# Kernel optimization log

Measured on AMD Instinct MI355X. Metric: run time of the kernel, lower is better.

The kernel has to match this reference:

```python
import jax, jax.numpy as jnp
import numpy as np

B, L, D = 8, 2048, 256
D_MODEL = 1024
NUM_SIGNALS = 16
MAX_POSITIONS = 4096
ROLE_OUTPUT = 2  # role id used for the CLS token


def setup_inputs() -> dict:
    key = jax.random.key(0)
    ks = jax.random.split(key, 12)
    emb = jax.random.normal(ks[0], (B, L, D), dtype=jnp.float32)
    pos = jax.random.randint(ks[1], (B, L), 1, MAX_POSITIONS + 1)          # pos >= 1 for real tokens
    sid = jax.random.randint(ks[2], (B, L), 0, NUM_SIGNALS)
    role = jax.random.randint(ks[3], (B, L), 0, 3)
    padding_mask = jax.random.uniform(ks[4], (B, L)) < 0.75                # True = real token
    # learned parameters
    proj_W = jax.random.normal(ks[5], (NUM_SIGNALS, D_MODEL, D), dtype=jnp.float32) * (1.0 / np.sqrt(D))
    proj_b = jax.random.normal(ks[6], (NUM_SIGNALS, D_MODEL), dtype=jnp.float32) * 0.01
    cls_content = jax.random.normal(ks[7], (D_MODEL,), dtype=jnp.float32)
    pos_embed = jax.random.normal(ks[8], (MAX_POSITIONS + 1, D_MODEL), dtype=jnp.float32)
    id_embed = jax.random.normal(ks[9], (NUM_SIGNALS + 1, D_MODEL), dtype=jnp.float32)
    role_embed = jax.random.normal(ks[10], (3, D_MODEL), dtype=jnp.float32)
    return dict(emb=emb, pos=pos, sid=sid, role=role, padding_mask=padding_mask,
                proj_W=proj_W, proj_b=proj_b, cls_content=cls_content,
                pos_embed=pos_embed, id_embed=id_embed, role_embed=role_embed)


def reference(emb, pos, sid, role, padding_mask,
              proj_W, proj_b, cls_content, pos_embed, id_embed, role_embed):
    Bv, Lv, _ = emb.shape
    S, d_model, _ = proj_W.shape
    cls_id = S

    # Grouped per-signal projection: one GEMM per signal id, select per token.
    tokens = jnp.zeros((Bv, Lv, d_model), dtype=emb.dtype)
    for s in range(S):
        proj_s = jnp.einsum('bld,ed->ble', emb, proj_W[s]) + proj_b[s]   # (B, L, d_model)
        keep = ((sid == s) & padding_mask)[..., None]
        tokens = jnp.where(keep, proj_s, tokens)

    # Prepend CLS
    cls = jnp.broadcast_to(cls_content[None, None, :], (Bv, 1, d_model))
    tokens = jnp.concatenate([cls, tokens], axis=1)                       # (B, L+1, d_model)

    pos_full = jnp.concatenate([jnp.zeros((Bv, 1), dtype=pos.dtype), pos], axis=1)
    sid_full = jnp.concatenate([jnp.full((Bv, 1), cls_id, dtype=sid.dtype), sid], axis=1)
    role_full = jnp.concatenate([jnp.full((Bv, 1), ROLE_OUTPUT, dtype=role.dtype), role], axis=1)

    tokens = tokens + pos_embed[pos_full] + id_embed[sid_full] + role_embed[role_full]

    attn_keep = jnp.concatenate([jnp.ones((Bv, 1), dtype=bool), padding_mask], axis=1)
    return tokens, attn_keep
```

## Files before the change

### kernel.cpp

```cpp
#include <hip/hip_runtime.h>
#include <hip/hip_bf16.h>
#include <stdint.h>

#define B_ 8
#define L_ 2048
#define NTOK 16384
#define DK 256
#define DM 1024
#define NS 16
#define LOUT 2049
#define TOK_OUT (B_*LOUT*DM)
#define ATTN_OUT (B_*LOUT)
#define PCAP 2048

typedef unsigned short u16;
typedef unsigned int u32;
typedef __bf16 bf16x8 __attribute__((ext_vector_type(8)));
typedef float f32x4 __attribute__((ext_vector_type(4)));

__device__ inline u32 packbf2(float lo, float hi) {
    u32 a, b;
    __builtin_memcpy(&a, &lo, 4);
    __builtin_memcpy(&b, &hi, 4);
    a = (a + 0x8000u) >> 16;
    b = (b + 0x8000u) & 0xFFFF0000u;
    return a | b;
}

__device__ inline void gll16(const void* g, void* l) {
    __builtin_amdgcn_global_load_lds(
        (const __attribute__((address_space(1))) unsigned int*)g,
        (__attribute__((address_space(3))) unsigned int*)l, 16, 0, 0);
}

#define WS_CUR 0
#define WS_PERM 64
#define EMB_OFF 262144ULL
#define W_OFF (EMB_OFF + 16384ULL * 512ULL)
#define WS_NEED (W_OFF + 16384ULL * 512ULL)

__device__ inline int sniff_width(const unsigned char* mb, int tid, int* sh) {
    if (tid == 0) { sh[0] = 0; sh[1] = 0; sh[2] = 0; }
    __syncthreads();
    int c1ge2 = 0, ge2 = 0, oddnz = 0;
    const u32* mw = (const u32*)mb;
    #pragma unroll
    for (int i = 0; i < 16; i++) {
        u32 x = mw[tid * 16 + i];
        u32 b0 = x & 0xFF, b1 = (x >> 8) & 0xFF, b2 = (x >> 16) & 0xFF, b3 = x >> 24;
        if (b1 >= 2) c1ge2 = 1;
        if (b0 >= 2 || b1 >= 2 || b2 >= 2 || b3 >= 2) ge2 = 1;
        if ((b1 | b3) != 0) oddnz = 1;
    }
    if (c1ge2) atomicOr(&sh[0], 1);
    if (ge2) atomicOr(&sh[1], 1);
    if (oddnz) atomicOr(&sh[2], 1);
    __syncthreads();
    if (sh[0]) return 2;
    if (sh[1]) return 4;
    if (sh[2]) return 1;
    return 4;
}

__device__ inline int decode_mask(const unsigned char* mb, int t, int width) {
    if (width == 1) return mb[t] != 0;
    if (width == 2) return ((const u16*)mb)[t] != 0;
    return ((const u32*)mb)[t] != 0;
}

#define SORT_B 64
#define CONV_B 2048
#define EW_B 4096
#define EW0 (SORT_B + CONV_B)
#define CLS0 (EW0 + EW_B)
#define ATTN0 (CLS0 + 2)
#define PREP_GRID (ATTN0 + 65)

__global__ __launch_bounds__(256) void prep_all(
    const unsigned char* __restrict__ mb, const int* __restrict__ sid,
    const int* __restrict__ pos, const int* __restrict__ role,
    const float* __restrict__ emb, const float* __restrict__ W,
    const float* __restrict__ cls, const float* __restrict__ pos_emb,
    const float* __restrict__ id_emb, const float* __restrict__ role_emb,
    int* __restrict__ wsi, unsigned char* __restrict__ wsb,
    float* __restrict__ out) {
    __shared__ int sh[3];
    __shared__ int lcnt[NS], gbase[NS];
    int bid = blockIdx.x;
    int tid = threadIdx.x;
    int lane = tid & 63;
    int wv = tid >> 6;

    if (bid < SORT_B) {
        if (tid < NS) lcnt[tid] = 0;
        int width = sniff_width(mb, tid, sh);
        int t = bid * 256 + tid;
        int m = decode_mask(mb, t, width);
        int s = sid[t];
        int lr = 0;
        if (m) lr = atomicAdd(&lcnt[s], 1);
        __syncthreads();
        if (tid < NS) gbase[tid] = atomicAdd(&wsi[WS_CUR + tid], lcnt[tid]);
        __syncthreads();
        if (m) {
            int r = gbase[s] + lr;
            if (r < PCAP) wsi[WS_PERM + s * PCAP + r] = t;
        }
        return;
    }

    if (bid < EW0) {
        int cb = bid - SORT_B;
        const float* src;
        u16* dst;
        if (cb < 1024) {
            src = emb;
            dst = (u16*)(wsb + EMB_OFF);
        } else {
            cb -= 1024;
            src = W;
            dst = (u16*)(wsb + W_OFF);
        }
        int r0 = cb * 16 + wv * 4;
        #pragma unroll
        for (int i = 0; i < 4; i++) {
            int r = r0 + i;
            float4 a = *(const float4*)(src + (size_t)r * DK + lane * 4);
            uint2 o;
            o.x = packbf2(a.x, a.y);
            o.y = packbf2(a.z, a.w);
            *(uint2*)(dst + (size_t)r * DK + lane * 4) = o;
        }
        return;
    }

    if (bid < CLS0) {
        int width = sniff_width(mb, tid, sh);
        int t = (bid - EW0) * 4 + wv;
        if (decode_mask(mb, t, width)) return;
        int p = pos[t], sd = sid[t], ro = role[t];
        int b = t >> 11, l = t & 2047;
        size_t orow = (size_t)(b * LOUT + l + 1) * DM;
        const float* pr = pos_emb + (size_t)p * DM;
        const float* ir = id_emb + (size_t)sd * DM;
        const float* rr = role_emb + (size_t)ro * DM;
        #pragma unroll
        for (int it = 0; it < 4; it++) {
            int c = it * 256 + lane * 4;
            f32x4 a = *(const f32x4*)(pr + c);
            f32x4 d = *(const f32x4*)(ir + c);
            f32x4 e = *(const f32x4*)(rr + c);
            f32x4 o = a + d + e;
            __builtin_nontemporal_store(o, (f32x4*)(out + orow + c));
        }
        return;
    }

    if (bid < ATTN0) {
        int b = (bid - CLS0) * 4 + wv;
        size_t orow = (size_t)(b * LOUT) * DM;
        #pragma unroll
        for (int it = 0; it < 4; it++) {
            int c = it * 256 + lane * 4;
            f32x4 cc = *(const f32x4*)(cls + c);
            f32x4 a = *(const f32x4*)(pos_emb + c);
            f32x4 d = *(const f32x4*)(id_emb + NS * DM + c);
            f32x4 e = *(const f32x4*)(role_emb + 2 * DM + c);
            f32x4 o = cc + a + d + e;
            *(f32x4*)(out + orow + c) = o;
        }
        return;
    }

    {
        int width = sniff_width(mb, tid, sh);
        int i = (bid - ATTN0) * 256 + tid;
        if (i < ATTN_OUT) {
            int b = i / LOUT;
            int j = i - b * LOUT;
            float val = (j == 0) ? 1.0f
                                 : (float)decode_mask(mb, b * L_ + j - 1, width);
            out[TOK_OUT + i] = val;
        }
    }
}

__global__ __launch_bounds__(512, 4) void gemm_big(
    const int* __restrict__ pos, const int* __restrict__ role,
    const float* __restrict__ bias,
    const float* __restrict__ pos_emb, const float* __restrict__ id_emb,
    const float* __restrict__ role_emb,
    const int* __restrict__ wsi, const unsigned char* __restrict__ wsb,
    float* __restrict__ out) {
    __shared__ u16 As[2][128 * 32];
    __shared__ u16 Bs[2][256 * 32];
    __shared__ int toks[128];
    int bi = (int)blockIdx.x;
    int tid = threadIdx.x;
    int lane = tid & 63;
    int wv = tid >> 6;

    int cnts[NS];
    int mtot = 0;
    #pragma unroll
    for (int i = 0; i < NS; i++) {
        int c = wsi[WS_CUR + i];
        cnts[i] = c > PCAP ? PCAP : c;
        mtot += (cnts[i] + 127) >> 7;
    }
    int xcd = bi & 7;
    int j = bi >> 3;
    int m_lo = (xcd * mtot) >> 3;
    int m_hi = ((xcd + 1) * mtot) >> 3;
    int cm = m_hi - m_lo;
    if (cm <= 0 || j >= cm * 4) return;
    int nt = j / cm;
    int m = m_lo + (j - nt * cm);
    int n0 = nt << 8;

    int s = -1, lrt = 0;
    #pragma unroll
    for (int i = 0; i < NS; i++) {
        int rt = (cnts[i] + 127) >> 7;
        if (s < 0) {
            if (m < rt) { s = i; lrt = m; }
            else m -= rt;
        }
    }
    if (s < 0) return;
    int rowsValid = cnts[s] - lrt * 128;
    if (rowsValid > 128) rowsValid = 128;

    if (tid < 128) {
        int base = WS_PERM + s * PCAP + lrt * 128;
        toks[tid] = wsi[base + ((tid < rowsValid) ? tid : 0)];
    }
    __syncthreads();

    const u16* Eb = (const u16*)(wsb + EMB_OFF);
    const u16* Bb = (const u16*)(wsb + W_OFF) + (size_t)(s * DM + n0) * DK;

    int srow = lane >> 2;
    int slseg = lane & 3;
    int arow = wv * 16 + srow;
    int ags = (slseg - (arow >> 1)) & 3;
    int brow1 = 128 + arow;
    int bgs1 = (slseg - (brow1 >> 1)) & 3;
    const u16* Asrc = Eb + (size_t)toks[arow] * DK;

    f32x4 acc[4][4];
    #pragma unroll
    for (int im = 0; im < 4; im++)
        #pragma unroll
        for (int jn = 0; jn < 4; jn++) acc[im][jn] = (f32x4){0.f, 0.f, 0.f, 0.f};

    int wm = wv & 1, wn = wv >> 1;
    int mcol = lane & 15;
    int quad = lane >> 4;

#define STAGE(kc, bf)                                                          \
    {                                                                          \
        gll16(Asrc + (kc) * 32 + ags * 8, &As[bf][wv * 16 * 32]);              \
        gll16(Bb + (size_t)arow * DK + (kc) * 32 + ags * 8,                    \
              &Bs[bf][wv * 16 * 32]);                                          \
        gll16(Bb + (size_t)brow1 * DK + (kc) * 32 + bgs1 * 8,                  \
              &Bs[bf][(128 + wv * 16) * 32]);                                  \
    }

    STAGE(0, 0)
    #pragma unroll
    for (int kc = 0; kc < 8; ++kc) {
        __syncthreads();
        if (kc < 7) STAGE(kc + 1, (kc + 1) & 1)
        int bf = kc & 1;
        bf16x8 af[4], bfr[4];
        #pragma unroll
        for (int im = 0; im < 4; im++) {
            int row = wm * 64 + im * 16 + mcol;
            int sg = (quad + (row >> 1)) & 3;
            af[im] = *(const bf16x8*)(&As[bf][row * 32 + sg * 8]);
        }
        #pragma unroll
        for (int jn = 0; jn < 4; jn++) {
            int row = wn * 64 + jn * 16 + mcol;
            int sg = (quad + (row >> 1)) & 3;
            bfr[jn] = *(const bf16x8*)(&Bs[bf][row * 32 + sg * 8]);
        }
        #pragma unroll
        for (int im = 0; im < 4; im++)
            #pragma unroll
            for (int jn = 0; jn < 4; jn++)
                acc[im][jn] = __builtin_amdgcn_mfma_f32_16x16x32_bf16(
                    af[im], bfr[jn], acc[im][jn], 0, 0, 0);
    }

    float bc[4];
    #pragma unroll
    for (int jn = 0; jn < 4; jn++) {
        int col = n0 + wn * 64 + jn * 16 + mcol;
        bc[jn] = bias[s * DM + col] + id_emb[s * DM + col];
    }
    #pragma unroll
    for (int im = 0; im < 4; im++) {
        #pragma unroll
        for (int r = 0; r < 4; r++) {
            int rowT = wm * 64 + im * 16 + quad * 4 + r;
            if (rowT >= rowsValid) continue;
            int t = toks[rowT];
            int p = pos[t];
            int ro = role[t];
            int b = t >> 11, l = t & 2047;
            size_t orow = (size_t)(b * LOUT + l + 1) * DM;
            const float* prow = pos_emb + (size_t)p * DM;
            #pragma unroll
            for (int jn = 0; jn < 4; jn++) {
                int col = n0 + wn * 64 + jn * 16 + mcol;
                float val = acc[im][jn][r] + bc[jn]
                    + prow[col]
                    + role_emb[ro * DM + col];
                __builtin_nontemporal_store(val, &out[orow + col]);
            }
        }
    }
#undef STAGE
}

extern "C" void kernel_launch(void* const* d_in, const int* in_sizes, int n_in,
                              void* d_out, int out_size, void* d_ws, size_t ws_size,
                              hipStream_t stream) {
    const float* emb = (const float*)d_in[0];
    const int* pos = (const int*)d_in[1];
    const int* sid = (const int*)d_in[2];
    const int* role = (const int*)d_in[3];
    const unsigned char* mask = (const unsigned char*)d_in[4];
    const float* W = (const float*)d_in[5];
    const float* bias = (const float*)d_in[6];
    const float* cls = (const float*)d_in[7];
    const float* pos_emb = (const float*)d_in[8];
    const float* id_emb = (const float*)d_in[9];
    const float* role_emb = (const float*)d_in[10];
    float* out = (float*)d_out;
    int* wsi = (int*)d_ws;
    unsigned char* wsb = (unsigned char*)d_ws;

    (void)hipMemsetAsync(wsi, 0, 64 * sizeof(int), stream);
    hipLaunchKernelGGL(prep_all, dim3(PREP_GRID), dim3(256), 0, stream,
                       mask, sid, pos, role, emb, W, cls, pos_emb, id_emb,
                       role_emb, wsi, wsb, out);
    hipLaunchKernelGGL(gemm_big, dim3(576), dim3(512), 0, stream,
                       pos, role, bias, pos_emb, id_emb, role_emb,
                       wsi, wsb, out);
}
```

Before: 156.6 us.

## Move unmasked-token, CLS and attn-mask writes from prep kernel into GEMM kernel tail

The sort phase now also builds a compacted list of padded (unmasked) token indices and records the detected mask width in the workspace. The elementwise writes for padded tokens, CLS rows and the attention mask move out of the prep kernel and into the tail of the GEMM kernel, which idle or finished GEMM blocks process in a grid-stride loop. The prep kernel shrinks to sorting plus bf16 conversion, now done with fewer, larger blocks of 64 rows each. The aim is to overlap the memory-bound embedding writes with the GEMM and shorten the prep critical path, at the cost of longer tails on GEMM blocks and a capacity limit (UCAP) on the padded-token list.

```diff
diff --git a/kernel.cpp b/kernel.cpp
--- a/kernel.cpp
+++ b/kernel.cpp
@@ -12,6 +12,7 @@
 #define TOK_OUT (B_*LOUT*DM)
 #define ATTN_OUT (B_*LOUT)
 #define PCAP 2048
+#define UCAP 8192
 
 typedef unsigned short u16;
 typedef unsigned int u32;
@@ -34,7 +35,10 @@
 }
 
 #define WS_CUR 0
+#define WS_UCUR 16
+#define WS_WIDTH 32
 #define WS_PERM 64
+#define WS_UNM (64 + NS * PCAP)
 #define EMB_OFF 262144ULL
 #define W_OFF (EMB_OFF + 16384ULL * 512ULL)
 #define WS_NEED (W_OFF + 16384ULL * 512ULL)
@@ -69,23 +73,15 @@
 }
 
 #define SORT_B 64
-#define CONV_B 2048
-#define EW_B 4096
-#define EW0 (SORT_B + CONV_B)
-#define CLS0 (EW0 + EW_B)
-#define ATTN0 (CLS0 + 2)
-#define PREP_GRID (ATTN0 + 65)
+#define PREP_GRID (SORT_B + 512)
 
 __global__ __launch_bounds__(256) void prep_all(
     const unsigned char* __restrict__ mb, const int* __restrict__ sid,
-    const int* __restrict__ pos, const int* __restrict__ role,
     const float* __restrict__ emb, const float* __restrict__ W,
-    const float* __restrict__ cls, const float* __restrict__ pos_emb,
-    const float* __restrict__ id_emb, const float* __restrict__ role_emb,
-    int* __restrict__ wsi, unsigned char* __restrict__ wsb,
-    float* __restrict__ out) {
+    int* __restrict__ wsi, unsigned char* __restrict__ wsb) {
     __shared__ int sh[3];
     __shared__ int lcnt[NS], gbase[NS];
+    __shared__ int lcnt_u, gbase_u;
     int bid = blockIdx.x;
     int tid = threadIdx.x;
     int lane = tid & 63;
@@ -93,101 +89,61 @@
 
     if (bid < SORT_B) {
         if (tid < NS) lcnt[tid] = 0;
+        if (tid == 0) lcnt_u = 0;
         int width = sniff_width(mb, tid, sh);
+        if (bid == 0 && tid == 0) wsi[WS_WIDTH] = width;
         int t = bid * 256 + tid;
         int m = decode_mask(mb, t, width);
         int s = sid[t];
-        int lr = 0;
+        int lr;
         if (m) lr = atomicAdd(&lcnt[s], 1);
+        else   lr = atomicAdd(&lcnt_u, 1);
         __syncthreads();
         if (tid < NS) gbase[tid] = atomicAdd(&wsi[WS_CUR + tid], lcnt[tid]);
+        if (tid == 0) gbase_u = atomicAdd(&wsi[WS_UCUR], lcnt_u);
         __syncthreads();
         if (m) {
             int r = gbase[s] + lr;
             if (r < PCAP) wsi[WS_PERM + s * PCAP + r] = t;
+        } else {
+            int r = gbase_u + lr;
+            if (r < UCAP) wsi[WS_UNM + r] = t;
         }
         return;
     }
 
-    if (bid < EW0) {
-        int cb = bid - SORT_B;
-        const float* src;
-        u16* dst;
-        if (cb < 1024) {
-            src = emb;
-            dst = (u16*)(wsb + EMB_OFF);
-        } else {
-            cb -= 1024;
-            src = W;
-            dst = (u16*)(wsb + W_OFF);
-        }
-        int r0 = cb * 16 + wv * 4;
-        #pragma unroll
-        for (int i = 0; i < 4; i++) {
-            int r = r0 + i;
-            float4 a = *(const float4*)(src + (size_t)r * DK + lane * 4);
-            uint2 o;
-            o.x = packbf2(a.x, a.y);
-            o.y = packbf2(a.z, a.w);
-            *(uint2*)(dst + (size_t)r * DK + lane * 4) = o;
-        }
-        return;
-    }
-
-    if (bid < CLS0) {
-        int width = sniff_width(mb, tid, sh);
-        int t = (bid - EW0) * 4 + wv;
-        if (decode_mask(mb, t, width)) return;
-        int p = pos[t], sd = sid[t], ro = role[t];
-        int b = t >> 11, l = t & 2047;
-        size_t orow = (size_t)(b * LOUT + l + 1) * DM;
-        const float* pr = pos_emb + (size_t)p * DM;
-        const float* ir = id_emb + (size_t)sd * DM;
-        const float* rr = role_emb + (size_t)ro * DM;
-        #pragma unroll
-        for (int it = 0; it < 4; it++) {
-            int c = it * 256 + lane * 4;
-            f32x4 a = *(const f32x4*)(pr + c);
-            f32x4 d = *(const f32x4*)(ir + c);
-            f32x4 e = *(const f32x4*)(rr + c);
-            f32x4 o = a + d + e;
-            __builtin_nontemporal_store(o, (f32x4*)(out + orow + c));
-        }
-        return;
-    }
-
-    if (bid < ATTN0) {
-        int b = (bid - CLS0) * 4 + wv;
-        size_t orow = (size_t)(b * LOUT) * DM;
-        #pragma unroll
-        for (int it = 0; it < 4; it++) {
-            int c = it * 256 + lane * 4;
-            f32x4 cc = *(const f32x4*)(cls + c);
-            f32x4 a = *(const f32x4*)(pos_emb + c);
-            f32x4 d = *(const f32x4*)(id_emb + NS * DM + c);
-            f32x4 e = *(const f32x4*)(role_emb + 2 * DM + c);
-            f32x4 o = cc + a + d + e;
-            *(f32x4*)(out + orow + c) = o;
-        }
-        return;
-    }
-
-    {
-        int width = sniff_width(mb, tid, sh);
-        int i = (bid - ATTN0) * 256 + tid;
-        if (i < ATTN_OUT) {
-            int b = i / LOUT;
-            int j = i - b * LOUT;
-            float val = (j == 0) ? 1.0f
-                                 : (float)decode_mask(mb, b * L_ + j - 1, width);
-            out[TOK_OUT + i] = val;
-        }
-    }
-}
+    int cb = bid - SORT_B;
+    const float* src;
+    u16* dst;
+    if (cb < 256) {
+        src = emb;
+        dst = (u16*)(wsb + EMB_OFF);
+    } else {
+        cb -= 256;
+        src = W;
+        dst = (u16*)(wsb + W_OFF);
+    }
+    int r0 = cb * 64 + wv * 16;
+    #pragma unroll 4
+    for (int i = 0; i < 16; i++) {
+        int r = r0 + i;
+        float4 a = *(const float4*)(src + (size_t)r * DK + lane * 4);
+        uint2 o;
+        o.x = packbf2(a.x, a.y);
+        o.y = packbf2(a.z, a.w);
+        *(uint2*)(dst + (size_t)r * DK + lane * 4) = o;
+    }
+}
+
+#define GEMM_GRID 576
+#define CLS_B0 535
+#define ATTN_B0 543
 
 __global__ __launch_bounds__(512, 4) void gemm_big(
-    const int* __restrict__ pos, const int* __restrict__ role,
-    const float* __restrict__ bias,
+    const unsigned char* __restrict__ mb,
+    const int* __restrict__ pos, const int* __restrict__ sid,
+    const int* __restrict__ role,
+    const float* __restrict__ bias, const float* __restrict__ cls,
     const float* __restrict__ pos_emb, const float* __restrict__ id_emb,
     const float* __restrict__ role_emb,
     const int* __restrict__ wsi, const unsigned char* __restrict__ wsb,
@@ -213,116 +169,169 @@
     int m_lo = (xcd * mtot) >> 3;
     int m_hi = ((xcd + 1) * mtot) >> 3;
     int cm = m_hi - m_lo;
-    if (cm <= 0 || j >= cm * 4) return;
-    int nt = j / cm;
-    int m = m_lo + (j - nt * cm);
-    int n0 = nt << 8;
-
-    int s = -1, lrt = 0;
-    #pragma unroll
-    for (int i = 0; i < NS; i++) {
-        int rt = (cnts[i] + 127) >> 7;
-        if (s < 0) {
-            if (m < rt) { s = i; lrt = m; }
-            else m -= rt;
-        }
-    }
-    if (s < 0) return;
-    int rowsValid = cnts[s] - lrt * 128;
-    if (rowsValid > 128) rowsValid = 128;
-
-    if (tid < 128) {
-        int base = WS_PERM + s * PCAP + lrt * 128;
-        toks[tid] = wsi[base + ((tid < rowsValid) ? tid : 0)];
-    }
-    __syncthreads();
-
-    const u16* Eb = (const u16*)(wsb + EMB_OFF);
-    const u16* Bb = (const u16*)(wsb + W_OFF) + (size_t)(s * DM + n0) * DK;
-
-    int srow = lane >> 2;
-    int slseg = lane & 3;
-    int arow = wv * 16 + srow;
-    int ags = (slseg - (arow >> 1)) & 3;
-    int brow1 = 128 + arow;
-    int bgs1 = (slseg - (brow1 >> 1)) & 3;
-    const u16* Asrc = Eb + (size_t)toks[arow] * DK;
-
-    f32x4 acc[4][4];
-    #pragma unroll
-    for (int im = 0; im < 4; im++)
-        #pragma unroll
-        for (int jn = 0; jn < 4; jn++) acc[im][jn] = (f32x4){0.f, 0.f, 0.f, 0.f};
-
-    int wm = wv & 1, wn = wv >> 1;
-    int mcol = lane & 15;
-    int quad = lane >> 4;
+    bool doGemm = (cm > 0 && j < cm * 4);
+    int s = -1, lrt = 0, n0 = 0;
+    if (doGemm) {
+        int nt = j / cm;
+        int m = m_lo + (j - nt * cm);
+        n0 = nt << 8;
+        #pragma unroll
+        for (int i = 0; i < NS; i++) {
+            int rt = (cnts[i] + 127) >> 7;
+            if (s < 0) {
+                if (m < rt) { s = i; lrt = m; }
+                else m -= rt;
+            }
+        }
+        if (s < 0) doGemm = false;
+    }
+
+    if (doGemm) {
+        int rowsValid = cnts[s] - lrt * 128;
+        if (rowsValid > 128) rowsValid = 128;
+
+        if (tid < 128) {
+            int base = WS_PERM + s * PCAP + lrt * 128;
+            toks[tid] = wsi[base + ((tid < rowsValid) ? tid : 0)];
+        }
+        __syncthreads();
+
+        const u16* Eb = (const u16*)(wsb + EMB_OFF);
+        const u16* Bb = (const u16*)(wsb + W_OFF) + (size_t)(s * DM + n0) * DK;
+
+        int srow = lane >> 2;
+        int slseg = lane & 3;
+        int arow = wv * 16 + srow;
+        int ags = (slseg - (arow >> 1)) & 3;
+        int brow1 = 128 + arow;
+        int bgs1 = (slseg - (brow1 >> 1)) & 3;
+        const u16* Asrc = Eb + (size_t)toks[arow] * DK;
+
+        f32x4 acc[4][4];
+        #pragma unroll
+        for (int im = 0; im < 4; im++)
+            #pragma unroll
+            for (int jn = 0; jn < 4; jn++) acc[im][jn] = (f32x4){0.f, 0.f, 0.f, 0.f};
+
+        int wm = wv & 1, wn = wv >> 1;
+        int mcol = lane & 15;
+        int quad = lane >> 4;
 
 #define STAGE(kc, bf)                                                          \
-    {                                                                          \
-        gll16(Asrc + (kc) * 32 + ags * 8, &As[bf][wv * 16 * 32]);              \
-        gll16(Bb + (size_t)arow * DK + (kc) * 32 + ags * 8,                    \
-              &Bs[bf][wv * 16 * 32]);                                          \
-        gll16(Bb + (size_t)brow1 * DK + (kc) * 32 + bgs1 * 8,                  \
-              &Bs[bf][(128 + wv * 16) * 32]);                                  \
-    }
-
-    STAGE(0, 0)
-    #pragma unroll
-    for (int kc = 0; kc < 8; ++kc) {
-        __syncthreads();
-        if (kc < 7) STAGE(kc + 1, (kc + 1) & 1)
-        int bf = kc & 1;
-        bf16x8 af[4], bfr[4];
+        {                                                                      \
+            gll16(Asrc + (kc) * 32 + ags * 8, &As[bf][wv * 16 * 32]);          \
+            gll16(Bb + (size_t)arow * DK + (kc) * 32 + ags * 8,                \
+                  &Bs[bf][wv * 16 * 32]);                                      \
+            gll16(Bb + (size_t)brow1 * DK + (kc) * 32 + bgs1 * 8,              \
+                  &Bs[bf][(128 + wv * 16) * 32]);                              \
+        }
+
+        STAGE(0, 0)
+        #pragma unroll
+        for (int kc = 0; kc < 8; ++kc) {
+            __syncthreads();
+            if (kc < 7) STAGE(kc + 1, (kc + 1) & 1)
+            int bf = kc & 1;
+            bf16x8 af[4], bfr[4];
+            #pragma unroll
+            for (int im = 0; im < 4; im++) {
+                int row = wm * 64 + im * 16 + mcol;
+                int sg = (quad + (row >> 1)) & 3;
+                af[im] = *(const bf16x8*)(&As[bf][row * 32 + sg * 8]);
+            }
+            #pragma unroll
+            for (int jn = 0; jn < 4; jn++) {
+                int row = wn * 64 + jn * 16 + mcol;
+                int sg = (quad + (row >> 1)) & 3;
+                bfr[jn] = *(const bf16x8*)(&Bs[bf][row * 32 + sg * 8]);
+            }
+            #pragma unroll
+            for (int im = 0; im < 4; im++)
+                #pragma unroll
+                for (int jn = 0; jn < 4; jn++)
+                    acc[im][jn] = __builtin_amdgcn_mfma_f32_16x16x32_bf16(
+                        af[im], bfr[jn], acc[im][jn], 0, 0, 0);
+        }
+#undef STAGE
+
+        float bc[4];
+        #pragma unroll
+        for (int jn = 0; jn < 4; jn++) {
+            int col = n0 + wn * 64 + jn * 16 + mcol;
+            bc[jn] = bias[s * DM + col] + id_emb[s * DM + col];
+        }
         #pragma unroll
         for (int im = 0; im < 4; im++) {
-            int row = wm * 64 + im * 16 + mcol;
-            int sg = (quad + (row >> 1)) & 3;
-            af[im] = *(const bf16x8*)(&As[bf][row * 32 + sg * 8]);
-        }
-        #pragma unroll
-        for (int jn = 0; jn < 4; jn++) {
-            int row = wn * 64 + jn * 16 + mcol;
-            int sg = (quad + (row >> 1)) & 3;
-            bfr[jn] = *(const bf16x8*)(&Bs[bf][row * 32 + sg * 8]);
-        }
-        #pragma unroll
-        for (int im = 0; im < 4; im++)
-            #pragma unroll
-            for (int jn = 0; jn < 4; jn++)
-                acc[im][jn] = __builtin_amdgcn_mfma_f32_16x16x32_bf16(
-                    af[im], bfr[jn], acc[im][jn], 0, 0, 0);
-    }
-
-    float bc[4];
-    #pragma unroll
-    for (int jn = 0; jn < 4; jn++) {
-        int col = n0 + wn * 64 + jn * 16 + mcol;
-        bc[jn] = bias[s * DM + col] + id_emb[s * DM + col];
-    }
-    #pragma unroll
-    for (int im = 0; im < 4; im++) {
-        #pragma unroll
-        for (int r = 0; r < 4; r++) {
-            int rowT = wm * 64 + im * 16 + quad * 4 + r;
-            if (rowT >= rowsValid) continue;
-            int t = toks[rowT];
-            int p = pos[t];
-            int ro = role[t];
+            #pragma unroll
+            for (int r = 0; r < 4; r++) {
+                int rowT = wm * 64 + im * 16 + quad * 4 + r;
+                if (rowT >= rowsValid) continue;
+                int t = toks[rowT];
+                int p = pos[t];
+                int ro = role[t];
+                int b = t >> 11, l = t & 2047;
+                size_t orow = (size_t)(b * LOUT + l + 1) * DM;
+                const float* prow = pos_emb + (size_t)p * DM;
+                #pragma unroll
+                for (int jn = 0; jn < 4; jn++) {
+                    int col = n0 + wn * 64 + jn * 16 + mcol;
+                    float val = acc[im][jn][r] + bc[jn]
+                        + prow[col]
+                        + role_emb[ro * DM + col];
+                    __builtin_nontemporal_store(val, &out[orow + col]);
+                }
+            }
+        }
+    }
+
+    {
+        int ucnt = wsi[WS_UCUR];
+        if (ucnt > UCAP) ucnt = UCAP;
+        for (int idx = (GEMM_GRID - 1 - bi) * 8 + wv; idx < ucnt;
+             idx += GEMM_GRID * 8) {
+            int t = wsi[WS_UNM + idx];
+            int p = pos[t], sd = sid[t], ro = role[t];
             int b = t >> 11, l = t & 2047;
             size_t orow = (size_t)(b * LOUT + l + 1) * DM;
-            const float* prow = pos_emb + (size_t)p * DM;
-            #pragma unroll
-            for (int jn = 0; jn < 4; jn++) {
-                int col = n0 + wn * 64 + jn * 16 + mcol;
-                float val = acc[im][jn][r] + bc[jn]
-                    + prow[col]
-                    + role_emb[ro * DM + col];
-                __builtin_nontemporal_store(val, &out[orow + col]);
-            }
-        }
-    }
-#undef STAGE
+            const float* pr = pos_emb + (size_t)p * DM;
+            const float* ir = id_emb + (size_t)sd * DM;
+            const float* rr = role_emb + (size_t)ro * DM;
+            #pragma unroll
+            for (int it = 0; it < 4; it++) {
+                int c = it * 256 + lane * 4;
+                f32x4 a = *(const f32x4*)(pr + c);
+                f32x4 d = *(const f32x4*)(ir + c);
+                f32x4 e = *(const f32x4*)(rr + c);
+                f32x4 o = a + d + e;
+                __builtin_nontemporal_store(o, (f32x4*)(out + orow + c));
+            }
+        }
+        if (bi >= CLS_B0 && bi < ATTN_B0 && wv == 0) {
+            int b = bi - CLS_B0;
+            size_t orow = (size_t)(b * LOUT) * DM;
+            #pragma unroll
+            for (int it = 0; it < 4; it++) {
+                int c = it * 256 + lane * 4;
+                f32x4 cc = *(const f32x4*)(cls + c);
+                f32x4 a = *(const f32x4*)(pos_emb + c);
+                f32x4 d = *(const f32x4*)(id_emb + NS * DM + c);
+                f32x4 e = *(const f32x4*)(role_emb + 2 * DM + c);
+                f32x4 o = cc + a + d + e;
+                *(f32x4*)(out + orow + c) = o;
+            }
+        }
+        if (bi >= ATTN_B0) {
+            int width = wsi[WS_WIDTH];
+            int i = (bi - ATTN_B0) * 512 + tid;
+            if (i < ATTN_OUT) {
+                int b = i / LOUT;
+                int jj = i - b * LOUT;
+                float val = (jj == 0) ? 1.0f
+                    : (float)decode_mask(mb, b * L_ + jj - 1, width);
+                out[TOK_OUT + i] = val;
+            }
+        }
+    }
 }
 
 extern "C" void kernel_launch(void* const* d_in, const int* in_sizes, int n_in,
@@ -345,9 +354,8 @@
 
     (void)hipMemsetAsync(wsi, 0, 64 * sizeof(int), stream);
     hipLaunchKernelGGL(prep_all, dim3(PREP_GRID), dim3(256), 0, stream,
-                       mask, sid, pos, role, emb, W, cls, pos_emb, id_emb,
+                       mask, sid, emb, W, wsi, wsb);
+    hipLaunchKernelGGL(gemm_big, dim3(GEMM_GRID), dim3(512), 0, stream,
+                       mask, pos, sid, role, bias, cls, pos_emb, id_emb,
                        role_emb, wsi, wsb, out);
-    hipLaunchKernelGGL(gemm_big, dim3(576), dim3(512), 0, stream,
-                       pos, role, bias, pos_emb, id_emb, role_emb,
-                       wsi, wsb, out);
-}
+}
```

New measurement: 157.7 us. About the same (+0.7%).
